# Performance work log

Hardware: AMD Instinct MI355X
Metric: run time of the kernel (lower is better)

Reference implementation:

```python
import jax, jax.numpy as jnp
import numpy as np

B, T, E, H = 4, 4096, 1024, 16
D = E // H          # per-head hidden_size in fla LinearAttention (num_heads=1)
CH = 64             # fused-chunk chunk size


def setup_inputs() -> dict:
    key = jax.random.key(0)
    k1, k2, k3, k4, k5 = jax.random.split(key, 5)
    s = 1.0 / np.sqrt(D).astype(np.float32)
    x = jax.random.normal(k1, (B, T, E), dtype=jnp.float32)
    Wq = jax.random.normal(k2, (D, D), dtype=jnp.float32) * s
    Wk = jax.random.normal(k3, (D, D), dtype=jnp.float32) * s
    Wv = jax.random.normal(k4, (D, D), dtype=jnp.float32) * s
    Wo = jax.random.normal(k5, (D, D), dtype=jnp.float32) * s
    return {"x": x, "Wq": Wq, "Wk": Wk, "Wv": Wv, "Wo": Wo}


def _phi(x):
    # fla 'elu' feature map: elu(x) + 1 (positive features)
    return jax.nn.elu(x) + 1.0


def _linear_attn_fused_chunk(q, k, v):
    # q,k,v: [B,H,T,D]; causal linear attention via chunked recurrence.
    b, h, t, d = q.shape
    n = t // CH
    # [N, B, H, CH, D] so scan runs over chunks
    qc = q.reshape(b, h, n, CH, d).transpose(2, 0, 1, 3, 4)
    kc = k.reshape(b, h, n, CH, d).transpose(2, 0, 1, 3, 4)
    vc = v.reshape(b, h, n, CH, d).transpose(2, 0, 1, 3, 4)
    mask = jnp.tril(jnp.ones((CH, CH), dtype=q.dtype))  # causal, diag inclusive

    def step(S, inp):
        qi, ki, vi = inp                                   # [B,H,CH,D]
        attn = jnp.einsum('bhck,bhek->bhce', qi, ki) * mask  # intra-chunk scores
        o_intra = jnp.einsum('bhce,bhed->bhcd', attn, vi)
        o_inter = jnp.einsum('bhck,bhkd->bhcd', qi, S)       # past-state term
        S_new = S + jnp.einsum('bhck,bhcd->bhkd', ki, vi)    # state update
        return S_new, o_intra + o_inter

    S0 = jnp.zeros((b, h, d, d), dtype=q.dtype)
    _, oc = jax.lax.scan(step, S0, (qc, kc, vc))           # oc: [N,B,H,CH,D]
    return oc.transpose(1, 2, 0, 3, 4).reshape(b, h, t, d)


def reference(x, Wq, Wk, Wv, Wo):
    # split outer heads: [B,T,E] -> [B,H,T,D]
    xh = x.reshape(B, T, H, D).transpose(0, 2, 1, 3)
    # shared [D,D] projections (fla LinearAttention with num_heads=1), tied elu feature map on q,k
    q = _phi(jnp.einsum('bhtd,de->bhte', xh, Wq))
    k = _phi(jnp.einsum('bhtd,de->bhte', xh, Wk))
    v = jnp.einsum('bhtd,de->bhte', xh, Wv)
    o = _linear_attn_fused_chunk(q, k, v)                  # no feature-map norm, identity output norm
    o = jnp.einsum('bhtd,de->bhte', o, Wo)
    return o.transpose(0, 2, 1, 3).reshape(B, T, E)
```

## Files before the change

kernel.cpp:

```cpp
#include <hip/hip_runtime.h>
#include <cstdint>
#include <cstddef>

constexpr int Bc = 4, Tc = 4096, Ec = 1024, Hc = 16, Dc = 64, CHc = 64;
constexpr int NSEG = 16;
constexpr int SEGT = Tc / NSEG;
constexpr int NCHUNK = SEGT / CHc;

typedef __attribute__((ext_vector_type(8))) short short8;
typedef __attribute__((ext_vector_type(4))) float f32x4;

__device__ __forceinline__ unsigned short* sws(unsigned short* b, int row, int colbyte) {
  return (unsigned short*)((char*)b + (row << 7) + (colbyte ^ ((row & 7) << 4)));
}

__device__ __forceinline__ unsigned short f2bf(float f) {
  union { float f; unsigned int u; } v; v.f = f;
  return (unsigned short)((v.u + 0x7FFFu + ((v.u >> 16) & 1u)) >> 16);
}
__device__ __forceinline__ unsigned int pk2(float lo, float hi) {
  union { float f; unsigned int u; } a, b; a.f = lo; b.f = hi;
  return ((a.u + 0x8000u) >> 16) | ((b.u + 0x8000u) & 0xFFFF0000u);
}
__device__ __forceinline__ float bf2f(unsigned short u) {
  union { unsigned int u; float f; } v; v.u = ((unsigned int)u) << 16;
  return v.f;
}
__device__ __forceinline__ float phi_elu1(float x) {
  return x > 0.f ? x + 1.f : __expf(x);
}
__device__ __forceinline__ short8 ld8(const unsigned short* p) {
  return *reinterpret_cast<const short8*>(p);
}
__device__ __forceinline__ short8 pk8(float4 a, float4 b) {
  union { unsigned int u[4]; short8 s; } r;
  r.u[0] = pk2(a.x, a.y); r.u[1] = pk2(a.z, a.w);
  r.u[2] = pk2(b.x, b.y); r.u[3] = pk2(b.z, b.w);
  return r.s;
}
__device__ __forceinline__ void st4(unsigned short* p, float v0, float v1, float v2, float v3) {
  uint2 t; t.x = pk2(v0, v1); t.y = pk2(v2, v3);
  *reinterpret_cast<uint2*>(p) = t;
}

#define MFMA(a, b, c) __builtin_amdgcn_mfma_f32_16x16x32_bf16((a), (b), (c), 0, 0, 0)

__global__ __launch_bounds__(256) void prep_weights(
    const float* __restrict__ Wq, const float* __restrict__ Wk,
    const float* __restrict__ Wv, const float* __restrict__ Wo,
    unsigned short* __restrict__ wbuf) {
  __shared__ float s_wvT[4096];
  __shared__ float s_wo[4096];
  const int tid = threadIdx.x;
  const int i = blockIdx.x * 256 + tid;
  for (int j = tid; j < 4096; j += 256) {
    s_wvT[(j & 63) * 64 + (j >> 6)] = Wv[j];
    s_wo[j] = Wo[j];
  }
  __syncthreads();
  const int r = i >> 6, c = i & 63;
  wbuf[c * 64 + r] = f2bf(Wq[i]);
  wbuf[4096 + c * 64 + r] = f2bf(Wk[i]);
  float acc = 0.f;
  for (int g = 0; g < 64; ++g)
    acc += s_wvT[g * 64 + c] * s_wo[g * 64 + r];
  wbuf[8192 + i] = f2bf(acc);
}

__global__ __launch_bounds__(256, 3) void pass1_kvseg(
    const float* __restrict__ x, const unsigned short* __restrict__ wbuf,
    float* __restrict__ kvseg) {
  __shared__ unsigned short s_kT[4096];
  __shared__ unsigned short s_vT[4096];
  const int tid = threadIdx.x, w = tid >> 6, lane = tid & 63, lr = lane & 15, lq = lane >> 4;
  const int bh = blockIdx.x, sg = blockIdx.y, b = bh >> 4, h = bh & 15;
  const float* xbase = x + ((size_t)b * Tc + (size_t)sg * SEGT) * Ec + h * Dc;
  const unsigned short* wkT = wbuf + 4096;
  const unsigned short* wvoT = wbuf + 8192;
  const f32x4 Z = {0.f, 0.f, 0.f, 0.f};

  short8 bwk[4][2], bwv[4][2];
#pragma unroll
  for (int c = 0; c < 4; ++c)
#pragma unroll
    for (int kk = 0; kk < 2; ++kk) {
      bwk[c][kk] = ld8(wkT + (c * 16 + lr) * 64 + kk * 32 + lq * 8);
      bwv[c][kk] = ld8(wvoT + (c * 16 + lr) * 64 + kk * 32 + lq * 8);
    }

  const float* xr = xbase + (size_t)(w * 16 + lr) * Ec + lq * 8;
  float4 p0 = ((const float4*)xr)[0], p1 = ((const float4*)xr)[1];
  float4 p2 = ((const float4*)(xr + 32))[0], p3 = ((const float4*)(xr + 32))[1];

  f32x4 sacc[4] = {Z, Z, Z, Z};
#pragma unroll
  for (int ci = 0; ci < NCHUNK; ++ci) {
    short8 xa0 = pk8(p0, p1), xa1 = pk8(p2, p3);
    if (ci < NCHUNK - 1) {
      const float* nr = xbase + (size_t)((ci + 1) * CHc + w * 16 + lr) * Ec + lq * 8;
      p0 = ((const float4*)nr)[0]; p1 = ((const float4*)nr)[1];
      p2 = ((const float4*)(nr + 32))[0]; p3 = ((const float4*)(nr + 32))[1];
    }
    f32x4 ak[4] = {Z, Z, Z, Z}, av[4] = {Z, Z, Z, Z};
#pragma unroll
    for (int c = 0; c < 4; ++c) {
      ak[c] = MFMA(xa0, bwk[c][0], ak[c]); ak[c] = MFMA(xa1, bwk[c][1], ak[c]);
      av[c] = MFMA(xa0, bwv[c][0], av[c]); av[c] = MFMA(xa1, bwv[c][1], av[c]);
    }
#pragma unroll
    for (int c = 0; c < 4; ++c) {
      unsigned short* pk_ = sws(s_kT, c * 16 + lr, w * 32 + lq * 8);
      unsigned short* pv_ = sws(s_vT, c * 16 + lr, w * 32 + lq * 8);
      st4(pk_, phi_elu1(ak[c][0]), phi_elu1(ak[c][1]), phi_elu1(ak[c][2]), phi_elu1(ak[c][3]));
      st4(pv_, av[c][0], av[c][1], av[c][2], av[c][3]);
    }
    __syncthreads();

    short8 akt0 = ld8(sws(s_kT, w * 16 + lr, lq * 16));
    short8 akt1 = ld8(sws(s_kT, w * 16 + lr, 64 + lq * 16));
#pragma unroll
    for (int c = 0; c < 4; ++c) {
      sacc[c] = MFMA(akt0, ld8(sws(s_vT, c * 16 + lr, lq * 16)), sacc[c]);
      sacc[c] = MFMA(akt1, ld8(sws(s_vT, c * 16 + lr, 64 + lq * 16)), sacc[c]);
    }
    __syncthreads();
  }
  float* dst = kvseg + ((size_t)(bh * NSEG + sg)) * 4096;
#pragma unroll
  for (int c = 0; c < 4; ++c)
#pragma unroll
    for (int j = 0; j < 4; ++j)
      dst[(w * 16 + lq * 4 + j) * 64 + c * 16 + lr] = sacc[c][j];
}

__global__ __launch_bounds__(256) void pass2_prefix(const float* __restrict__ kvseg,
                                                    unsigned short* __restrict__ sprefix) {
  const int bh = blockIdx.x, tile = blockIdx.y;
  const int e = tile * 1024 + threadIdx.x * 4;
  const float* src = kvseg + (size_t)bh * NSEG * 4096 + e;
  unsigned short* dst = sprefix + (size_t)bh * NSEG * 4096 + e;
  float4 vals[NSEG];
#pragma unroll
  for (int s = 0; s < NSEG; ++s) vals[s] = *(const float4*)(src + (size_t)s * 4096);
  float a0 = 0.f, a1 = 0.f, a2 = 0.f, a3 = 0.f;
#pragma unroll
  for (int s = 0; s < NSEG; ++s) {
    uint2 t; t.x = pk2(a0, a1); t.y = pk2(a2, a3);
    *reinterpret_cast<uint2*>(dst + (size_t)s * 4096) = t;
    a0 += vals[s].x; a1 += vals[s].y; a2 += vals[s].z; a3 += vals[s].w;
  }
}

__global__ __launch_bounds__(256, 2) void pass3_main(
    const float* __restrict__ x, const unsigned short* __restrict__ wbuf,
    const unsigned short* __restrict__ sprefix, float* __restrict__ out) {
  __shared__ unsigned short s_x [4096];
  __shared__ unsigned short s_q [4096];
  __shared__ unsigned short s_k [4096];
  __shared__ unsigned short s_kT[4096];
  __shared__ unsigned short s_vT[4096];
  __shared__ unsigned short s_Sb[4096];

  const int tid = threadIdx.x, w = tid >> 6, lane = tid & 63, lr = lane & 15, lq = lane >> 4;
  const int bh = blockIdx.x, sg = blockIdx.y, b = bh >> 4, h = bh & 15;
  const float* xbase = x + ((size_t)b * Tc + (size_t)sg * SEGT) * Ec + h * Dc;
  float* obase = out + ((size_t)b * Tc + (size_t)sg * SEGT) * Ec + h * Dc;
  const unsigned short* wqT = wbuf;
  const unsigned short* wkT = wbuf + 4096;
  const unsigned short* wvoT = wbuf + 8192;
  const unsigned short* Sg = sprefix + ((size_t)(bh * NSEG + sg)) * 4096;
  const int sr = tid >> 2, sc = tid & 3;
  const f32x4 Z = {0.f, 0.f, 0.f, 0.f};

  f32x4 sacc[4];
#pragma unroll
  for (int c = 0; c < 4; ++c)
#pragma unroll
    for (int j = 0; j < 4; ++j)
      sacc[c][j] = bf2f(Sg[(w * 16 + lq * 4 + j) * 64 + c * 16 + lr]);

  short8 awq[2], awk[2], bwk[4][2], bwv[4][2];
#pragma unroll
  for (int kk = 0; kk < 2; ++kk) {
    awq[kk] = ld8(wqT + (w * 16 + lr) * 64 + kk * 32 + lq * 8);
    awk[kk] = ld8(wkT + (w * 16 + lr) * 64 + kk * 32 + lq * 8);
  }
#pragma unroll
  for (int c = 0; c < 4; ++c)
#pragma unroll
    for (int kk = 0; kk < 2; ++kk) {
      bwk[c][kk] = ld8(wkT + (c * 16 + lr) * 64 + kk * 32 + lq * 8);
      bwv[c][kk] = ld8(wvoT + (c * 16 + lr) * 64 + kk * 32 + lq * 8);
    }

  {
    const float4* xf = (const float4*)(xbase + (size_t)sr * Ec + sc * 16);
    float4 f0 = xf[0], f1 = xf[1], f2 = xf[2], f3 = xf[3];
    *(short8*)sws(s_x, sr, sc * 32) = pk8(f0, f1);
    *(short8*)sws(s_x, sr, sc * 32 + 16) = pk8(f2, f3);
  }
  __syncthreads();

#pragma unroll
  for (int ci = 0; ci < NCHUNK; ++ci) {
    float4 pf0, pf1, pf2, pf3;
    if (ci < NCHUNK - 1) {
      const float4* xf = (const float4*)(xbase + (size_t)((ci + 1) * CHc + sr) * Ec + sc * 16);
      pf0 = xf[0]; pf1 = xf[1]; pf2 = xf[2]; pf3 = xf[3];
    }

    short8 xb[4][2];
#pragma unroll
    for (int c = 0; c < 4; ++c) {
      xb[c][0] = ld8(sws(s_x, c * 16 + lr, lq * 16));
      xb[c][1] = ld8(sws(s_x, c * 16 + lr, 64 + lq * 16));
    }
    short8 xw0 = ld8(sws(s_x, w * 16 + lr, lq * 16));
    short8 xw1 = ld8(sws(s_x, w * 16 + lr, 64 + lq * 16));
#pragma unroll
    for (int c = 0; c < 4; ++c)
      st4(sws(s_Sb, c * 16 + lr, w * 32 + lq * 8), sacc[c][0], sacc[c][1], sacc[c][2], sacc[c][3]);

    f32x4 aqt[4] = {Z, Z, Z, Z}, akt[4] = {Z, Z, Z, Z}, ack[4] = {Z, Z, Z, Z}, acv[4] = {Z, Z, Z, Z};
#pragma unroll
    for (int c = 0; c < 4; ++c) {
      aqt[c] = MFMA(awq[0], xb[c][0], aqt[c]); aqt[c] = MFMA(awq[1], xb[c][1], aqt[c]);
      akt[c] = MFMA(awk[0], xb[c][0], akt[c]); akt[c] = MFMA(awk[1], xb[c][1], akt[c]);
      ack[c] = MFMA(xw0, bwk[c][0], ack[c]);   ack[c] = MFMA(xw1, bwk[c][1], ack[c]);
      acv[c] = MFMA(xw0, bwv[c][0], acv[c]);   acv[c] = MFMA(xw1, bwv[c][1], acv[c]);
    }
#pragma unroll
    for (int c = 0; c < 4; ++c) {
      const int row = c * 16 + lr, cb = w * 32 + lq * 8;
      st4(sws(s_q, row, cb), phi_elu1(aqt[c][0]), phi_elu1(aqt[c][1]), phi_elu1(aqt[c][2]), phi_elu1(aqt[c][3]));
      st4(sws(s_k, row, cb), phi_elu1(akt[c][0]), phi_elu1(akt[c][1]), phi_elu1(akt[c][2]), phi_elu1(akt[c][3]));
      st4(sws(s_kT, row, cb), phi_elu1(ack[c][0]), phi_elu1(ack[c][1]), phi_elu1(ack[c][2]), phi_elu1(ack[c][3]));
      st4(sws(s_vT, row, cb), acv[c][0], acv[c][1], acv[c][2], acv[c][3]);
    }
    __syncthreads();

    short8 a_q0 = ld8(sws(s_q, w * 16 + lr, lq * 16));
    short8 a_q1 = ld8(sws(s_q, w * 16 + lr, 64 + lq * 16));
    short8 a_k0 = ld8(sws(s_k, w * 16 + lr, lq * 16));
    short8 a_k1 = ld8(sws(s_k, w * 16 + lr, 64 + lq * 16));
    short8 a_t0 = ld8(sws(s_kT, w * 16 + lr, lq * 16));
    short8 a_t1 = ld8(sws(s_kT, w * 16 + lr, 64 + lq * 16));
    f32x4 aat[4] = {Z, Z, Z, Z}, ao[4] = {Z, Z, Z, Z};
#pragma unroll
    for (int c = 0; c < 4; ++c) {
      const int row = c * 16 + lr;
      aat[c]  = MFMA(a_k0, ld8(sws(s_q, row, lq * 16)), aat[c]);
      aat[c]  = MFMA(a_k1, ld8(sws(s_q, row, 64 + lq * 16)), aat[c]);
      ao[c]   = MFMA(a_q0, ld8(sws(s_Sb, row, lq * 16)), ao[c]);
      ao[c]   = MFMA(a_q1, ld8(sws(s_Sb, row, 64 + lq * 16)), ao[c]);
      sacc[c] = MFMA(a_t0, ld8(sws(s_vT, row, lq * 16)), sacc[c]);
      sacc[c] = MFMA(a_t1, ld8(sws(s_vT, row, 64 + lq * 16)), sacc[c]);
    }
#pragma unroll
    for (int c = 0; c < 4; ++c) {
      int t = c * 16 + lr, tp = w * 16 + lq * 4;
      float m0 = (tp + 0 <= t) ? aat[c][0] : 0.f;
      float m1 = (tp + 1 <= t) ? aat[c][1] : 0.f;
      float m2 = (tp + 2 <= t) ? aat[c][2] : 0.f;
      float m3 = (tp + 3 <= t) ? aat[c][3] : 0.f;
      st4(sws(s_x, t, tp * 2), m0, m1, m2, m3);
    }
    __syncthreads();

    short8 a_a0 = ld8(sws(s_x, w * 16 + lr, lq * 16));
    short8 a_a1 = ld8(sws(s_x, w * 16 + lr, 64 + lq * 16));
#pragma unroll
    for (int c = 0; c < 4; ++c) {
      const int row = c * 16 + lr;
      ao[c] = MFMA(a_a0, ld8(sws(s_vT, row, lq * 16)), ao[c]);
      ao[c] = MFMA(a_a1, ld8(sws(s_vT, row, 64 + lq * 16)), ao[c]);
    }
    float* orow = obase + (size_t)(ci * CHc) * Ec;
#pragma unroll
    for (int c = 0; c < 4; ++c)
#pragma unroll
      for (int j = 0; j < 4; ++j)
        orow[(size_t)(w * 16 + lq * 4 + j) * Ec + c * 16 + lr] = ao[c][j];
    if (ci < NCHUNK - 1) {
      *(short8*)sws(s_x, sr, sc * 32) = pk8(pf0, pf1);
      *(short8*)sws(s_x, sr, sc * 32 + 16) = pk8(pf2, pf3);
    }
    __syncthreads();
  }
}

extern "C" void kernel_launch(void* const* d_in, const int* in_sizes, int n_in,
                              void* d_out, int out_size, void* d_ws, size_t ws_size,
                              hipStream_t stream) {
  const float* x  = (const float*)d_in[0];
  const float* Wq = (const float*)d_in[1];
  const float* Wk = (const float*)d_in[2];
  const float* Wv = (const float*)d_in[3];
  const float* Wo = (const float*)d_in[4];
  float* out = (float*)d_out;

  unsigned short* wbuf = (unsigned short*)d_ws;
  float* kvseg = (float*)((char*)d_ws + 32768);
  unsigned short* sprefix = (unsigned short*)((char*)d_ws + 32768 + (size_t)16 * 1024 * 1024);

  prep_weights<<<dim3(16), dim3(256), 0, stream>>>(Wq, Wk, Wv, Wo, wbuf);
  pass1_kvseg<<<dim3(64, NSEG), dim3(256), 0, stream>>>(x, wbuf, kvseg);
  pass2_prefix<<<dim3(64, 4), dim3(256), 0, stream>>>(kvseg, sprefix);
  pass3_main<<<dim3(64, NSEG), dim3(256), 0, stream>>>(x, wbuf, sprefix, out);
}
```

Measured before the change: 77.56 us.

## Split pass1 into half-segment blocks, double pass3 waves, store kv partials in bf16

Pass1 now computes KV partial sums over two-chunk half-segments (32 per head) and stores them in bf16 with a transposed layout. Pass2 reads these bf16 partials and writes the prefix only at even indices. Pass3 runs with 512 threads, each wave covering half the column tiles, and double-buffers the x tile in shared memory. It also loads fewer weight fragments per thread. The aim is more parallelism and less partial-sum traffic, at the cost of bf16 rounding in the partials and extra LDS use.

```diff
diff --git a/kernel.cpp b/kernel.cpp
--- a/kernel.cpp
+++ b/kernel.cpp
@@ -6,6 +6,7 @@
 constexpr int NSEG = 16;
 constexpr int SEGT = Tc / NSEG;
 constexpr int NCHUNK = SEGT / CHc;
+constexpr int NHALF = 32;
 
 typedef __attribute__((ext_vector_type(8))) short short8;
 typedef __attribute__((ext_vector_type(4))) float f32x4;
@@ -20,10 +21,10 @@
 }
 __device__ __forceinline__ unsigned int pk2(float lo, float hi) {
   union { float f; unsigned int u; } a, b; a.f = lo; b.f = hi;
-  return ((a.u + 0x8000u) >> 16) | ((b.u + 0x8000u) & 0xFFFF0000u);
-}
-__device__ __forceinline__ float bf2f(unsigned short u) {
-  union { unsigned int u; float f; } v; v.u = ((unsigned int)u) << 16;
+  return __builtin_amdgcn_perm(b.u + 0x8000u, a.u + 0x8000u, 0x07060302u);
+}
+__device__ __forceinline__ float bf2f(unsigned int u16) {
+  union { unsigned int u; float f; } v; v.u = u16 << 16;
   return v.f;
 }
 __device__ __forceinline__ float phi_elu1(float x) {
@@ -67,14 +68,14 @@
   wbuf[8192 + i] = f2bf(acc);
 }
 
-__global__ __launch_bounds__(256, 3) void pass1_kvseg(
+__global__ __launch_bounds__(256, 3) void pass1_kvhalf(
     const float* __restrict__ x, const unsigned short* __restrict__ wbuf,
-    float* __restrict__ kvseg) {
+    unsigned short* __restrict__ kvh) {
   __shared__ unsigned short s_kT[4096];
   __shared__ unsigned short s_vT[4096];
   const int tid = threadIdx.x, w = tid >> 6, lane = tid & 63, lr = lane & 15, lq = lane >> 4;
-  const int bh = blockIdx.x, sg = blockIdx.y, b = bh >> 4, h = bh & 15;
-  const float* xbase = x + ((size_t)b * Tc + (size_t)sg * SEGT) * Ec + h * Dc;
+  const int bh = blockIdx.x, hs = blockIdx.y, b = bh >> 4, h = bh & 15;
+  const float* xbase = x + ((size_t)b * Tc + (size_t)hs * 2 * CHc) * Ec + h * Dc;
   const unsigned short* wkT = wbuf + 4096;
   const unsigned short* wvoT = wbuf + 8192;
   const f32x4 Z = {0.f, 0.f, 0.f, 0.f};
@@ -94,10 +95,10 @@
 
   f32x4 sacc[4] = {Z, Z, Z, Z};
 #pragma unroll
-  for (int ci = 0; ci < NCHUNK; ++ci) {
+  for (int ci = 0; ci < 2; ++ci) {
     short8 xa0 = pk8(p0, p1), xa1 = pk8(p2, p3);
-    if (ci < NCHUNK - 1) {
-      const float* nr = xbase + (size_t)((ci + 1) * CHc + w * 16 + lr) * Ec + lq * 8;
+    if (ci == 0) {
+      const float* nr = xbase + (size_t)(CHc + w * 16 + lr) * Ec + lq * 8;
       p0 = ((const float4*)nr)[0]; p1 = ((const float4*)nr)[1];
       p2 = ((const float4*)(nr + 32))[0]; p3 = ((const float4*)(nr + 32))[1];
     }
@@ -109,13 +110,11 @@
     }
 #pragma unroll
     for (int c = 0; c < 4; ++c) {
-      unsigned short* pk_ = sws(s_kT, c * 16 + lr, w * 32 + lq * 8);
-      unsigned short* pv_ = sws(s_vT, c * 16 + lr, w * 32 + lq * 8);
-      st4(pk_, phi_elu1(ak[c][0]), phi_elu1(ak[c][1]), phi_elu1(ak[c][2]), phi_elu1(ak[c][3]));
-      st4(pv_, av[c][0], av[c][1], av[c][2], av[c][3]);
-    }
-    __syncthreads();
-
+      st4(sws(s_kT, c * 16 + lr, w * 32 + lq * 8),
+          phi_elu1(ak[c][0]), phi_elu1(ak[c][1]), phi_elu1(ak[c][2]), phi_elu1(ak[c][3]));
+      st4(sws(s_vT, c * 16 + lr, w * 32 + lq * 8), av[c][0], av[c][1], av[c][2], av[c][3]);
+    }
+    __syncthreads();
     short8 akt0 = ld8(sws(s_kT, w * 16 + lr, lq * 16));
     short8 akt1 = ld8(sws(s_kT, w * 16 + lr, 64 + lq * 16));
 #pragma unroll
@@ -125,36 +124,39 @@
     }
     __syncthreads();
   }
-  float* dst = kvseg + ((size_t)(bh * NSEG + sg)) * 4096;
-#pragma unroll
-  for (int c = 0; c < 4; ++c)
-#pragma unroll
-    for (int j = 0; j < 4; ++j)
-      dst[(w * 16 + lq * 4 + j) * 64 + c * 16 + lr] = sacc[c][j];
-}
-
-__global__ __launch_bounds__(256) void pass2_prefix(const float* __restrict__ kvseg,
-                                                    unsigned short* __restrict__ sprefix) {
+  unsigned short* dst = kvh + ((size_t)bh * NHALF + hs) * 4096;
+#pragma unroll
+  for (int c = 0; c < 4; ++c) {
+    uint2 t; t.x = pk2(sacc[c][0], sacc[c][1]); t.y = pk2(sacc[c][2], sacc[c][3]);
+    *reinterpret_cast<uint2*>(dst + (c * 16 + lr) * 64 + w * 16 + lq * 4) = t;
+  }
+}
+
+__global__ __launch_bounds__(256) void pass2_prefix(const unsigned short* __restrict__ kvh,
+                                                    unsigned short* __restrict__ spre) {
   const int bh = blockIdx.x, tile = blockIdx.y;
-  const int e = tile * 1024 + threadIdx.x * 4;
-  const float* src = kvseg + (size_t)bh * NSEG * 4096 + e;
-  unsigned short* dst = sprefix + (size_t)bh * NSEG * 4096 + e;
-  float4 vals[NSEG];
-#pragma unroll
-  for (int s = 0; s < NSEG; ++s) vals[s] = *(const float4*)(src + (size_t)s * 4096);
+  const int e4 = tile * 1024 + threadIdx.x * 4;
+  const unsigned short* src = kvh + (size_t)bh * NHALF * 4096 + e4;
+  unsigned short* dst = spre + (size_t)bh * NSEG * 4096 + e4;
+  uint2 vals[NHALF];
+#pragma unroll
+  for (int s = 0; s < NHALF; ++s) vals[s] = *(const uint2*)(src + (size_t)s * 4096);
   float a0 = 0.f, a1 = 0.f, a2 = 0.f, a3 = 0.f;
 #pragma unroll
-  for (int s = 0; s < NSEG; ++s) {
-    uint2 t; t.x = pk2(a0, a1); t.y = pk2(a2, a3);
-    *reinterpret_cast<uint2*>(dst + (size_t)s * 4096) = t;
-    a0 += vals[s].x; a1 += vals[s].y; a2 += vals[s].z; a3 += vals[s].w;
-  }
-}
-
-__global__ __launch_bounds__(256, 2) void pass3_main(
+  for (int s = 0; s < NHALF; ++s) {
+    if ((s & 1) == 0) {
+      uint2 t; t.x = pk2(a0, a1); t.y = pk2(a2, a3);
+      *reinterpret_cast<uint2*>(dst + (size_t)(s >> 1) * 4096) = t;
+    }
+    a0 += bf2f(vals[s].x & 0xFFFFu); a1 += bf2f(vals[s].x >> 16);
+    a2 += bf2f(vals[s].y & 0xFFFFu); a3 += bf2f(vals[s].y >> 16);
+  }
+}
+
+__global__ __launch_bounds__(512, 2) void pass3_main(
     const float* __restrict__ x, const unsigned short* __restrict__ wbuf,
-    const unsigned short* __restrict__ sprefix, float* __restrict__ out) {
-  __shared__ unsigned short s_x [4096];
+    const unsigned short* __restrict__ spre, float* __restrict__ out) {
+  __shared__ unsigned short s_xb[2][4096];
   __shared__ unsigned short s_q [4096];
   __shared__ unsigned short s_k [4096];
   __shared__ unsigned short s_kT[4096];
@@ -162,129 +164,137 @@
   __shared__ unsigned short s_Sb[4096];
 
   const int tid = threadIdx.x, w = tid >> 6, lane = tid & 63, lr = lane & 15, lq = lane >> 4;
+  const int wr = w & 3, wc = w >> 2;
+  const int sr8 = tid >> 3, sc8 = tid & 7;
   const int bh = blockIdx.x, sg = blockIdx.y, b = bh >> 4, h = bh & 15;
   const float* xbase = x + ((size_t)b * Tc + (size_t)sg * SEGT) * Ec + h * Dc;
   float* obase = out + ((size_t)b * Tc + (size_t)sg * SEGT) * Ec + h * Dc;
   const unsigned short* wqT = wbuf;
   const unsigned short* wkT = wbuf + 4096;
   const unsigned short* wvoT = wbuf + 8192;
-  const unsigned short* Sg = sprefix + ((size_t)(bh * NSEG + sg)) * 4096;
-  const int sr = tid >> 2, sc = tid & 3;
+  const unsigned short* SgT = spre + ((size_t)(bh * NSEG + sg)) * 4096;
   const f32x4 Z = {0.f, 0.f, 0.f, 0.f};
 
-  f32x4 sacc[4];
-#pragma unroll
-  for (int c = 0; c < 4; ++c)
-#pragma unroll
-    for (int j = 0; j < 4; ++j)
-      sacc[c][j] = bf2f(Sg[(w * 16 + lq * 4 + j) * 64 + c * 16 + lr]);
-
-  short8 awq[2], awk[2], bwk[4][2], bwv[4][2];
+  const int rA = wr * 16 + lr;
+  const int r0 = (2 * wc) * 16 + lr;
+  const int r1 = (2 * wc + 1) * 16 + lr;
+
+  f32x4 sacc[2];
+  {
+    uint2 u0 = *(const uint2*)(SgT + r0 * 64 + wr * 16 + lq * 4);
+    uint2 u1 = *(const uint2*)(SgT + r1 * 64 + wr * 16 + lq * 4);
+    sacc[0][0] = bf2f(u0.x & 0xFFFFu); sacc[0][1] = bf2f(u0.x >> 16);
+    sacc[0][2] = bf2f(u0.y & 0xFFFFu); sacc[0][3] = bf2f(u0.y >> 16);
+    sacc[1][0] = bf2f(u1.x & 0xFFFFu); sacc[1][1] = bf2f(u1.x >> 16);
+    sacc[1][2] = bf2f(u1.y & 0xFFFFu); sacc[1][3] = bf2f(u1.y >> 16);
+  }
+
+  short8 awq[2], awk[2], bwk[2][2], bwv[2][2];
 #pragma unroll
   for (int kk = 0; kk < 2; ++kk) {
-    awq[kk] = ld8(wqT + (w * 16 + lr) * 64 + kk * 32 + lq * 8);
-    awk[kk] = ld8(wkT + (w * 16 + lr) * 64 + kk * 32 + lq * 8);
-  }
-#pragma unroll
-  for (int c = 0; c < 4; ++c)
+    awq[kk] = ld8(wqT + rA * 64 + kk * 32 + lq * 8);
+    awk[kk] = ld8(wkT + rA * 64 + kk * 32 + lq * 8);
+    bwk[0][kk] = ld8(wkT + r0 * 64 + kk * 32 + lq * 8);
+    bwk[1][kk] = ld8(wkT + r1 * 64 + kk * 32 + lq * 8);
+    bwv[0][kk] = ld8(wvoT + r0 * 64 + kk * 32 + lq * 8);
+    bwv[1][kk] = ld8(wvoT + r1 * 64 + kk * 32 + lq * 8);
+  }
+
+  {
+    const float4* xf = (const float4*)(xbase + (size_t)sr8 * Ec + sc8 * 8);
+    *(short8*)sws(s_xb[0], sr8, sc8 * 16) = pk8(xf[0], xf[1]);
+  }
+  __syncthreads();
+
+#pragma unroll
+  for (int ci = 0; ci < NCHUNK; ++ci) {
+    unsigned short* cur = s_xb[ci & 1];
+    unsigned short* nxt = s_xb[(ci & 1) ^ 1];
+
+    short8 xb0[2], xb1[2], xw[2];
 #pragma unroll
     for (int kk = 0; kk < 2; ++kk) {
-      bwk[c][kk] = ld8(wkT + (c * 16 + lr) * 64 + kk * 32 + lq * 8);
-      bwv[c][kk] = ld8(wvoT + (c * 16 + lr) * 64 + kk * 32 + lq * 8);
-    }
-
-  {
-    const float4* xf = (const float4*)(xbase + (size_t)sr * Ec + sc * 16);
-    float4 f0 = xf[0], f1 = xf[1], f2 = xf[2], f3 = xf[3];
-    *(short8*)sws(s_x, sr, sc * 32) = pk8(f0, f1);
-    *(short8*)sws(s_x, sr, sc * 32 + 16) = pk8(f2, f3);
-  }
-  __syncthreads();
-
-#pragma unroll
-  for (int ci = 0; ci < NCHUNK; ++ci) {
-    float4 pf0, pf1, pf2, pf3;
+      xb0[kk] = ld8(sws(cur, r0, kk * 64 + lq * 16));
+      xb1[kk] = ld8(sws(cur, r1, kk * 64 + lq * 16));
+      xw[kk]  = ld8(sws(cur, rA, kk * 64 + lq * 16));
+    }
+    st4(sws(s_Sb, r0, wr * 32 + lq * 8), sacc[0][0], sacc[0][1], sacc[0][2], sacc[0][3]);
+    st4(sws(s_Sb, r1, wr * 32 + lq * 8), sacc[1][0], sacc[1][1], sacc[1][2], sacc[1][3]);
+
+    f32x4 aqt[2] = {Z, Z}, akt[2] = {Z, Z}, ack[2] = {Z, Z}, acv[2] = {Z, Z};
+    aqt[0] = MFMA(awq[0], xb0[0], aqt[0]); aqt[0] = MFMA(awq[1], xb0[1], aqt[0]);
+    aqt[1] = MFMA(awq[0], xb1[0], aqt[1]); aqt[1] = MFMA(awq[1], xb1[1], aqt[1]);
+    akt[0] = MFMA(awk[0], xb0[0], akt[0]); akt[0] = MFMA(awk[1], xb0[1], akt[0]);
+    akt[1] = MFMA(awk[0], xb1[0], akt[1]); akt[1] = MFMA(awk[1], xb1[1], akt[1]);
+    ack[0] = MFMA(xw[0], bwk[0][0], ack[0]); ack[0] = MFMA(xw[1], bwk[0][1], ack[0]);
+    ack[1] = MFMA(xw[0], bwk[1][0], ack[1]); ack[1] = MFMA(xw[1], bwk[1][1], ack[1]);
+    acv[0] = MFMA(xw[0], bwv[0][0], acv[0]); acv[0] = MFMA(xw[1], bwv[0][1], acv[0]);
+    acv[1] = MFMA(xw[0], bwv[1][0], acv[1]); acv[1] = MFMA(xw[1], bwv[1][1], acv[1]);
+
+#pragma unroll
+    for (int c2 = 0; c2 < 2; ++c2) {
+      const int row = c2 ? r1 : r0, cb = wr * 32 + lq * 8;
+      st4(sws(s_q, row, cb), phi_elu1(aqt[c2][0]), phi_elu1(aqt[c2][1]), phi_elu1(aqt[c2][2]), phi_elu1(aqt[c2][3]));
+      st4(sws(s_k, row, cb), phi_elu1(akt[c2][0]), phi_elu1(akt[c2][1]), phi_elu1(akt[c2][2]), phi_elu1(akt[c2][3]));
+      st4(sws(s_kT, row, cb), phi_elu1(ack[c2][0]), phi_elu1(ack[c2][1]), phi_elu1(ack[c2][2]), phi_elu1(ack[c2][3]));
+      st4(sws(s_vT, row, cb), acv[c2][0], acv[c2][1], acv[c2][2], acv[c2][3]);
+    }
+    __syncthreads();
+
+    float4 pf0, pf1;
     if (ci < NCHUNK - 1) {
-      const float4* xf = (const float4*)(xbase + (size_t)((ci + 1) * CHc + sr) * Ec + sc * 16);
-      pf0 = xf[0]; pf1 = xf[1]; pf2 = xf[2]; pf3 = xf[3];
-    }
-
-    short8 xb[4][2];
-#pragma unroll
-    for (int c = 0; c < 4; ++c) {
-      xb[c][0] = ld8(sws(s_x, c * 16 + lr, lq * 16));
-      xb[c][1] = ld8(sws(s_x, c * 16 + lr, 64 + lq * 16));
-    }
-    short8 xw0 = ld8(sws(s_x, w * 16 + lr, lq * 16));
-    short8 xw1 = ld8(sws(s_x, w * 16 + lr, 64 + lq * 16));
-#pragma unroll
-    for (int c = 0; c < 4; ++c)
-      st4(sws(s_Sb, c * 16 + lr, w * 32 + lq * 8), sacc[c][0], sacc[c][1], sacc[c][2], sacc[c][3]);
-
-    f32x4 aqt[4] = {Z, Z, Z, Z}, akt[4] = {Z, Z, Z, Z}, ack[4] = {Z, Z, Z, Z}, acv[4] = {Z, Z, Z, Z};
-#pragma unroll
-    for (int c = 0; c < 4; ++c) {
-      aqt[c] = MFMA(awq[0], xb[c][0], aqt[c]); aqt[c] = MFMA(awq[1], xb[c][1], aqt[c]);
-      akt[c] = MFMA(awk[0], xb[c][0], akt[c]); akt[c] = MFMA(awk[1], xb[c][1], akt[c]);
-      ack[c] = MFMA(xw0, bwk[c][0], ack[c]);   ack[c] = MFMA(xw1, bwk[c][1], ack[c]);
-      acv[c] = MFMA(xw0, bwv[c][0], acv[c]);   acv[c] = MFMA(xw1, bwv[c][1], acv[c]);
-    }
-#pragma unroll
-    for (int c = 0; c < 4; ++c) {
-      const int row = c * 16 + lr, cb = w * 32 + lq * 8;
-      st4(sws(s_q, row, cb), phi_elu1(aqt[c][0]), phi_elu1(aqt[c][1]), phi_elu1(aqt[c][2]), phi_elu1(aqt[c][3]));
-      st4(sws(s_k, row, cb), phi_elu1(akt[c][0]), phi_elu1(akt[c][1]), phi_elu1(akt[c][2]), phi_elu1(akt[c][3]));
-      st4(sws(s_kT, row, cb), phi_elu1(ack[c][0]), phi_elu1(ack[c][1]), phi_elu1(ack[c][2]), phi_elu1(ack[c][3]));
-      st4(sws(s_vT, row, cb), acv[c][0], acv[c][1], acv[c][2], acv[c][3]);
-    }
-    __syncthreads();
-
-    short8 a_q0 = ld8(sws(s_q, w * 16 + lr, lq * 16));
-    short8 a_q1 = ld8(sws(s_q, w * 16 + lr, 64 + lq * 16));
-    short8 a_k0 = ld8(sws(s_k, w * 16 + lr, lq * 16));
-    short8 a_k1 = ld8(sws(s_k, w * 16 + lr, 64 + lq * 16));
-    short8 a_t0 = ld8(sws(s_kT, w * 16 + lr, lq * 16));
-    short8 a_t1 = ld8(sws(s_kT, w * 16 + lr, 64 + lq * 16));
-    f32x4 aat[4] = {Z, Z, Z, Z}, ao[4] = {Z, Z, Z, Z};
-#pragma unroll
-    for (int c = 0; c < 4; ++c) {
-      const int row = c * 16 + lr;
-      aat[c]  = MFMA(a_k0, ld8(sws(s_q, row, lq * 16)), aat[c]);
-      aat[c]  = MFMA(a_k1, ld8(sws(s_q, row, 64 + lq * 16)), aat[c]);
-      ao[c]   = MFMA(a_q0, ld8(sws(s_Sb, row, lq * 16)), ao[c]);
-      ao[c]   = MFMA(a_q1, ld8(sws(s_Sb, row, 64 + lq * 16)), ao[c]);
-      sacc[c] = MFMA(a_t0, ld8(sws(s_vT, row, lq * 16)), sacc[c]);
-      sacc[c] = MFMA(a_t1, ld8(sws(s_vT, row, 64 + lq * 16)), sacc[c]);
-    }
-#pragma unroll
-    for (int c = 0; c < 4; ++c) {
-      int t = c * 16 + lr, tp = w * 16 + lq * 4;
-      float m0 = (tp + 0 <= t) ? aat[c][0] : 0.f;
-      float m1 = (tp + 1 <= t) ? aat[c][1] : 0.f;
-      float m2 = (tp + 2 <= t) ? aat[c][2] : 0.f;
-      float m3 = (tp + 3 <= t) ? aat[c][3] : 0.f;
-      st4(sws(s_x, t, tp * 2), m0, m1, m2, m3);
-    }
-    __syncthreads();
-
-    short8 a_a0 = ld8(sws(s_x, w * 16 + lr, lq * 16));
-    short8 a_a1 = ld8(sws(s_x, w * 16 + lr, 64 + lq * 16));
-#pragma unroll
-    for (int c = 0; c < 4; ++c) {
-      const int row = c * 16 + lr;
-      ao[c] = MFMA(a_a0, ld8(sws(s_vT, row, lq * 16)), ao[c]);
-      ao[c] = MFMA(a_a1, ld8(sws(s_vT, row, 64 + lq * 16)), ao[c]);
+      const float4* xf = (const float4*)(xbase + (size_t)((ci + 1) * CHc + sr8) * Ec + sc8 * 8);
+      pf0 = xf[0]; pf1 = xf[1];
+    }
+
+    short8 aq[2], ak2[2], at[2];
+#pragma unroll
+    for (int kk = 0; kk < 2; ++kk) {
+      aq[kk]  = ld8(sws(s_q, rA, kk * 64 + lq * 16));
+      ak2[kk] = ld8(sws(s_k, rA, kk * 64 + lq * 16));
+      at[kk]  = ld8(sws(s_kT, rA, kk * 64 + lq * 16));
+    }
+    f32x4 aat[2] = {Z, Z}, ao[2] = {Z, Z};
+#pragma unroll
+    for (int c2 = 0; c2 < 2; ++c2) {
+      const int row = c2 ? r1 : r0;
+      aat[c2]  = MFMA(ak2[0], ld8(sws(s_q, row, lq * 16)), aat[c2]);
+      aat[c2]  = MFMA(ak2[1], ld8(sws(s_q, row, 64 + lq * 16)), aat[c2]);
+      ao[c2]   = MFMA(aq[0], ld8(sws(s_Sb, row, lq * 16)), ao[c2]);
+      ao[c2]   = MFMA(aq[1], ld8(sws(s_Sb, row, 64 + lq * 16)), ao[c2]);
+      sacc[c2] = MFMA(at[0], ld8(sws(s_vT, row, lq * 16)), sacc[c2]);
+      sacc[c2] = MFMA(at[1], ld8(sws(s_vT, row, 64 + lq * 16)), sacc[c2]);
+    }
+#pragma unroll
+    for (int c2 = 0; c2 < 2; ++c2) {
+      const int t = c2 ? r1 : r0, tp = wr * 16 + lq * 4;
+      float m0 = (tp + 0 <= t) ? aat[c2][0] : 0.f;
+      float m1 = (tp + 1 <= t) ? aat[c2][1] : 0.f;
+      float m2 = (tp + 2 <= t) ? aat[c2][2] : 0.f;
+      float m3 = (tp + 3 <= t) ? aat[c2][3] : 0.f;
+      st4(sws(cur, t, tp * 2), m0, m1, m2, m3);
+    }
+    __syncthreads();
+
+    short8 aa[2];
+    aa[0] = ld8(sws(cur, rA, lq * 16));
+    aa[1] = ld8(sws(cur, rA, 64 + lq * 16));
+#pragma unroll
+    for (int c2 = 0; c2 < 2; ++c2) {
+      const int row = c2 ? r1 : r0;
+      ao[c2] = MFMA(aa[0], ld8(sws(s_vT, row, lq * 16)), ao[c2]);
+      ao[c2] = MFMA(aa[1], ld8(sws(s_vT, row, 64 + lq * 16)), ao[c2]);
     }
     float* orow = obase + (size_t)(ci * CHc) * Ec;
 #pragma unroll
-    for (int c = 0; c < 4; ++c)
+    for (int c2 = 0; c2 < 2; ++c2) {
+      const int col = c2 ? r1 : r0;
 #pragma unroll
       for (int j = 0; j < 4; ++j)
-        orow[(size_t)(w * 16 + lq * 4 + j) * Ec + c * 16 + lr] = ao[c][j];
-    if (ci < NCHUNK - 1) {
-      *(short8*)sws(s_x, sr, sc * 32) = pk8(pf0, pf1);
-      *(short8*)sws(s_x, sr, sc * 32 + 16) = pk8(pf2, pf3);
-    }
+        orow[(size_t)(wr * 16 + lq * 4 + j) * Ec + col] = ao[c2][j];
+    }
+    if (ci < NCHUNK - 1)
+      *(short8*)sws(nxt, sr8, sc8 * 16) = pk8(pf0, pf1);
     __syncthreads();
   }
 }
@@ -300,11 +310,11 @@
   float* out = (float*)d_out;
 
   unsigned short* wbuf = (unsigned short*)d_ws;
-  float* kvseg = (float*)((char*)d_ws + 32768);
-  unsigned short* sprefix = (unsigned short*)((char*)d_ws + 32768 + (size_t)16 * 1024 * 1024);
+  unsigned short* kvh  = (unsigned short*)((char*)d_ws + 32768);
+  unsigned short* spre = (unsigned short*)((char*)d_ws + 32768 + (size_t)16 * 1024 * 1024);
 
   prep_weights<<<dim3(16), dim3(256), 0, stream>>>(Wq, Wk, Wv, Wo, wbuf);
-  pass1_kvseg<<<dim3(64, NSEG), dim3(256), 0, stream>>>(x, wbuf, kvseg);
-  pass2_prefix<<<dim3(64, 4), dim3(256), 0, stream>>>(kvseg, sprefix);
-  pass3_main<<<dim3(64, NSEG), dim3(256), 0, stream>>>(x, wbuf, sprefix, out);
-}
+  pass1_kvhalf<<<dim3(64, NHALF), dim3(256), 0, stream>>>(x, wbuf, kvh);
+  pass2_prefix<<<dim3(64, 4), dim3(256), 0, stream>>>(kvh, spre);
+  pass3_main<<<dim3(64, NSEG), dim3(512), 0, stream>>>(x, wbuf, spre, out);
+}
```

New measurement: 89.13 us. 14.9% more time.

## Compute per-chunk KV states in pass1 and scan them in bf16 prefix pass

Applied to the files above, without the earlier changes.

Pass1 now launches one block per 64-token chunk instead of per 256-token segment, so there is no serial chunk loop and the grid is four times larger. It writes each chunk's K^T V state as bf16 in a register-fragment layout. Pass2 scans all 64 chunk states, emitting bf16 segment prefixes, and pass3 reads them with vectorized loads in that fragment layout. The diff also adds s_setprio around the MFMA blocks in pass3 and a perm-based bf16 pack; bf16 storage of the per-chunk partials adds rounding error to the accumulation.

```diff
diff --git a/kernel.cpp b/kernel.cpp
--- a/kernel.cpp
+++ b/kernel.cpp
@@ -6,6 +6,7 @@
 constexpr int NSEG = 16;
 constexpr int SEGT = Tc / NSEG;
 constexpr int NCHUNK = SEGT / CHc;
+constexpr int NCH = Tc / CHc;
 
 typedef __attribute__((ext_vector_type(8))) short short8;
 typedef __attribute__((ext_vector_type(4))) float f32x4;
@@ -20,10 +21,10 @@
 }
 __device__ __forceinline__ unsigned int pk2(float lo, float hi) {
   union { float f; unsigned int u; } a, b; a.f = lo; b.f = hi;
-  return ((a.u + 0x8000u) >> 16) | ((b.u + 0x8000u) & 0xFFFF0000u);
-}
-__device__ __forceinline__ float bf2f(unsigned short u) {
-  union { unsigned int u; float f; } v; v.u = ((unsigned int)u) << 16;
+  return __builtin_amdgcn_perm(b.u + 0x8000u, a.u + 0x8000u, 0x07060302u);
+}
+__device__ __forceinline__ float bf2f(unsigned int u16) {
+  union { unsigned int u; float f; } v; v.u = u16 << 16;
   return v.f;
 }
 __device__ __forceinline__ float phi_elu1(float x) {
@@ -67,14 +68,14 @@
   wbuf[8192 + i] = f2bf(acc);
 }
 
-__global__ __launch_bounds__(256, 3) void pass1_kvseg(
+__global__ __launch_bounds__(256, 3) void pass1_kvchunk(
     const float* __restrict__ x, const unsigned short* __restrict__ wbuf,
-    float* __restrict__ kvseg) {
+    unsigned short* __restrict__ kvc) {
   __shared__ unsigned short s_kT[4096];
   __shared__ unsigned short s_vT[4096];
   const int tid = threadIdx.x, w = tid >> 6, lane = tid & 63, lr = lane & 15, lq = lane >> 4;
-  const int bh = blockIdx.x, sg = blockIdx.y, b = bh >> 4, h = bh & 15;
-  const float* xbase = x + ((size_t)b * Tc + (size_t)sg * SEGT) * Ec + h * Dc;
+  const int bh = blockIdx.x, ch = blockIdx.y, b = bh >> 4, h = bh & 15;
+  const float* xbase = x + ((size_t)b * Tc + (size_t)ch * CHc) * Ec + h * Dc;
   const unsigned short* wkT = wbuf + 4096;
   const unsigned short* wvoT = wbuf + 8192;
   const f32x4 Z = {0.f, 0.f, 0.f, 0.f};
@@ -91,69 +92,68 @@
   const float* xr = xbase + (size_t)(w * 16 + lr) * Ec + lq * 8;
   float4 p0 = ((const float4*)xr)[0], p1 = ((const float4*)xr)[1];
   float4 p2 = ((const float4*)(xr + 32))[0], p3 = ((const float4*)(xr + 32))[1];
-
+  short8 xa0 = pk8(p0, p1), xa1 = pk8(p2, p3);
+
+  f32x4 ak[4] = {Z, Z, Z, Z}, av[4] = {Z, Z, Z, Z};
+#pragma unroll
+  for (int c = 0; c < 4; ++c) {
+    ak[c] = MFMA(xa0, bwk[c][0], ak[c]); ak[c] = MFMA(xa1, bwk[c][1], ak[c]);
+    av[c] = MFMA(xa0, bwv[c][0], av[c]); av[c] = MFMA(xa1, bwv[c][1], av[c]);
+  }
+#pragma unroll
+  for (int c = 0; c < 4; ++c) {
+    st4(sws(s_kT, c * 16 + lr, w * 32 + lq * 8),
+        phi_elu1(ak[c][0]), phi_elu1(ak[c][1]), phi_elu1(ak[c][2]), phi_elu1(ak[c][3]));
+    st4(sws(s_vT, c * 16 + lr, w * 32 + lq * 8), av[c][0], av[c][1], av[c][2], av[c][3]);
+  }
+  __syncthreads();
+
+  short8 akt0 = ld8(sws(s_kT, w * 16 + lr, lq * 16));
+  short8 akt1 = ld8(sws(s_kT, w * 16 + lr, 64 + lq * 16));
   f32x4 sacc[4] = {Z, Z, Z, Z};
 #pragma unroll
-  for (int ci = 0; ci < NCHUNK; ++ci) {
-    short8 xa0 = pk8(p0, p1), xa1 = pk8(p2, p3);
-    if (ci < NCHUNK - 1) {
-      const float* nr = xbase + (size_t)((ci + 1) * CHc + w * 16 + lr) * Ec + lq * 8;
-      p0 = ((const float4*)nr)[0]; p1 = ((const float4*)nr)[1];
-      p2 = ((const float4*)(nr + 32))[0]; p3 = ((const float4*)(nr + 32))[1];
-    }
-    f32x4 ak[4] = {Z, Z, Z, Z}, av[4] = {Z, Z, Z, Z};
-#pragma unroll
-    for (int c = 0; c < 4; ++c) {
-      ak[c] = MFMA(xa0, bwk[c][0], ak[c]); ak[c] = MFMA(xa1, bwk[c][1], ak[c]);
-      av[c] = MFMA(xa0, bwv[c][0], av[c]); av[c] = MFMA(xa1, bwv[c][1], av[c]);
-    }
-#pragma unroll
-    for (int c = 0; c < 4; ++c) {
-      unsigned short* pk_ = sws(s_kT, c * 16 + lr, w * 32 + lq * 8);
-      unsigned short* pv_ = sws(s_vT, c * 16 + lr, w * 32 + lq * 8);
-      st4(pk_, phi_elu1(ak[c][0]), phi_elu1(ak[c][1]), phi_elu1(ak[c][2]), phi_elu1(ak[c][3]));
-      st4(pv_, av[c][0], av[c][1], av[c][2], av[c][3]);
-    }
-    __syncthreads();
-
-    short8 akt0 = ld8(sws(s_kT, w * 16 + lr, lq * 16));
-    short8 akt1 = ld8(sws(s_kT, w * 16 + lr, 64 + lq * 16));
-#pragma unroll
-    for (int c = 0; c < 4; ++c) {
-      sacc[c] = MFMA(akt0, ld8(sws(s_vT, c * 16 + lr, lq * 16)), sacc[c]);
-      sacc[c] = MFMA(akt1, ld8(sws(s_vT, c * 16 + lr, 64 + lq * 16)), sacc[c]);
-    }
-    __syncthreads();
-  }
-  float* dst = kvseg + ((size_t)(bh * NSEG + sg)) * 4096;
-#pragma unroll
-  for (int c = 0; c < 4; ++c)
-#pragma unroll
-    for (int j = 0; j < 4; ++j)
-      dst[(w * 16 + lq * 4 + j) * 64 + c * 16 + lr] = sacc[c][j];
-}
-
-__global__ __launch_bounds__(256) void pass2_prefix(const float* __restrict__ kvseg,
-                                                    unsigned short* __restrict__ sprefix) {
-  const int bh = blockIdx.x, tile = blockIdx.y;
-  const int e = tile * 1024 + threadIdx.x * 4;
-  const float* src = kvseg + (size_t)bh * NSEG * 4096 + e;
-  unsigned short* dst = sprefix + (size_t)bh * NSEG * 4096 + e;
-  float4 vals[NSEG];
-#pragma unroll
-  for (int s = 0; s < NSEG; ++s) vals[s] = *(const float4*)(src + (size_t)s * 4096);
+  for (int c = 0; c < 4; ++c) {
+    sacc[c] = MFMA(akt0, ld8(sws(s_vT, c * 16 + lr, lq * 16)), sacc[c]);
+    sacc[c] = MFMA(akt1, ld8(sws(s_vT, c * 16 + lr, 64 + lq * 16)), sacc[c]);
+  }
+
+  unsigned short* dst = kvc + ((size_t)bh * NCH + ch) * 4096 + (w * 64 + lane) * 16;
+#pragma unroll
+  for (int c = 0; c < 4; ++c) {
+    uint2 t; t.x = pk2(sacc[c][0], sacc[c][1]); t.y = pk2(sacc[c][2], sacc[c][3]);
+    *reinterpret_cast<uint2*>(dst + c * 4) = t;
+  }
+}
+
+__global__ __launch_bounds__(256) void pass2_prefix(const unsigned short* __restrict__ kvc,
+                                                    unsigned short* __restrict__ spre) {
+  const int bh = blockIdx.x, tb = blockIdx.y;
+  const int slot = tb * 256 + threadIdx.x;
+  const unsigned short* src = kvc + (size_t)bh * NCH * 4096 + slot * 4;
+  unsigned short* dst = spre + (size_t)bh * NSEG * 4096 + slot * 4;
   float a0 = 0.f, a1 = 0.f, a2 = 0.f, a3 = 0.f;
 #pragma unroll
-  for (int s = 0; s < NSEG; ++s) {
-    uint2 t; t.x = pk2(a0, a1); t.y = pk2(a2, a3);
-    *reinterpret_cast<uint2*>(dst + (size_t)s * 4096) = t;
-    a0 += vals[s].x; a1 += vals[s].y; a2 += vals[s].z; a3 += vals[s].w;
+  for (int base = 0; base < NCH; base += 8) {
+    uint2 v[8];
+#pragma unroll
+    for (int i = 0; i < 8; ++i)
+      v[i] = *reinterpret_cast<const uint2*>(src + (size_t)(base + i) * 4096);
+#pragma unroll
+    for (int i = 0; i < 8; ++i) {
+      const int c = base + i;
+      if ((c & 3) == 0) {
+        uint2 t; t.x = pk2(a0, a1); t.y = pk2(a2, a3);
+        *reinterpret_cast<uint2*>(dst + (size_t)(c >> 2) * 4096) = t;
+      }
+      a0 += bf2f(v[i].x & 0xFFFFu); a1 += bf2f(v[i].x >> 16);
+      a2 += bf2f(v[i].y & 0xFFFFu); a3 += bf2f(v[i].y >> 16);
+    }
   }
 }
 
 __global__ __launch_bounds__(256, 2) void pass3_main(
     const float* __restrict__ x, const unsigned short* __restrict__ wbuf,
-    const unsigned short* __restrict__ sprefix, float* __restrict__ out) {
+    const unsigned short* __restrict__ spre, float* __restrict__ out) {
   __shared__ unsigned short s_x [4096];
   __shared__ unsigned short s_q [4096];
   __shared__ unsigned short s_k [4096];
@@ -168,16 +168,19 @@
   const unsigned short* wqT = wbuf;
   const unsigned short* wkT = wbuf + 4096;
   const unsigned short* wvoT = wbuf + 8192;
-  const unsigned short* Sg = sprefix + ((size_t)(bh * NSEG + sg)) * 4096;
   const int sr = tid >> 2, sc = tid & 3;
   const f32x4 Z = {0.f, 0.f, 0.f, 0.f};
 
   f32x4 sacc[4];
-#pragma unroll
-  for (int c = 0; c < 4; ++c)
-#pragma unroll
-    for (int j = 0; j < 4; ++j)
-      sacc[c][j] = bf2f(Sg[(w * 16 + lq * 4 + j) * 64 + c * 16 + lr]);
+  {
+    const unsigned short* Sg = spre + ((size_t)(bh * NSEG + sg)) * 4096 + (w * 64 + lane) * 16;
+#pragma unroll
+    for (int c = 0; c < 4; ++c) {
+      uint2 u = *reinterpret_cast<const uint2*>(Sg + c * 4);
+      sacc[c][0] = bf2f(u.x & 0xFFFFu); sacc[c][1] = bf2f(u.x >> 16);
+      sacc[c][2] = bf2f(u.y & 0xFFFFu); sacc[c][3] = bf2f(u.y >> 16);
+    }
+  }
 
   short8 awq[2], awk[2], bwk[4][2], bwv[4][2];
 #pragma unroll
@@ -222,6 +225,7 @@
       st4(sws(s_Sb, c * 16 + lr, w * 32 + lq * 8), sacc[c][0], sacc[c][1], sacc[c][2], sacc[c][3]);
 
     f32x4 aqt[4] = {Z, Z, Z, Z}, akt[4] = {Z, Z, Z, Z}, ack[4] = {Z, Z, Z, Z}, acv[4] = {Z, Z, Z, Z};
+    __builtin_amdgcn_s_setprio(1);
 #pragma unroll
     for (int c = 0; c < 4; ++c) {
       aqt[c] = MFMA(awq[0], xb[c][0], aqt[c]); aqt[c] = MFMA(awq[1], xb[c][1], aqt[c]);
@@ -229,6 +233,7 @@
       ack[c] = MFMA(xw0, bwk[c][0], ack[c]);   ack[c] = MFMA(xw1, bwk[c][1], ack[c]);
       acv[c] = MFMA(xw0, bwv[c][0], acv[c]);   acv[c] = MFMA(xw1, bwv[c][1], acv[c]);
     }
+    __builtin_amdgcn_s_setprio(0);
 #pragma unroll
     for (int c = 0; c < 4; ++c) {
       const int row = c * 16 + lr, cb = w * 32 + lq * 8;
@@ -246,6 +251,7 @@
     short8 a_t0 = ld8(sws(s_kT, w * 16 + lr, lq * 16));
     short8 a_t1 = ld8(sws(s_kT, w * 16 + lr, 64 + lq * 16));
     f32x4 aat[4] = {Z, Z, Z, Z}, ao[4] = {Z, Z, Z, Z};
+    __builtin_amdgcn_s_setprio(1);
 #pragma unroll
     for (int c = 0; c < 4; ++c) {
       const int row = c * 16 + lr;
@@ -256,6 +262,7 @@
       sacc[c] = MFMA(a_t0, ld8(sws(s_vT, row, lq * 16)), sacc[c]);
       sacc[c] = MFMA(a_t1, ld8(sws(s_vT, row, 64 + lq * 16)), sacc[c]);
     }
+    __builtin_amdgcn_s_setprio(0);
 #pragma unroll
     for (int c = 0; c < 4; ++c) {
       int t = c * 16 + lr, tp = w * 16 + lq * 4;
@@ -269,12 +276,14 @@
 
     short8 a_a0 = ld8(sws(s_x, w * 16 + lr, lq * 16));
     short8 a_a1 = ld8(sws(s_x, w * 16 + lr, 64 + lq * 16));
+    __builtin_amdgcn_s_setprio(1);
 #pragma unroll
     for (int c = 0; c < 4; ++c) {
       const int row = c * 16 + lr;
       ao[c] = MFMA(a_a0, ld8(sws(s_vT, row, lq * 16)), ao[c]);
       ao[c] = MFMA(a_a1, ld8(sws(s_vT, row, 64 + lq * 16)), ao[c]);
     }
+    __builtin_amdgcn_s_setprio(0);
     float* orow = obase + (size_t)(ci * CHc) * Ec;
 #pragma unroll
     for (int c = 0; c < 4; ++c)
@@ -300,11 +309,11 @@
   float* out = (float*)d_out;
 
   unsigned short* wbuf = (unsigned short*)d_ws;
-  float* kvseg = (float*)((char*)d_ws + 32768);
-  unsigned short* sprefix = (unsigned short*)((char*)d_ws + 32768 + (size_t)16 * 1024 * 1024);
+  unsigned short* kvc  = (unsigned short*)((char*)d_ws + 32768);
+  unsigned short* spre = (unsigned short*)((char*)d_ws + 32768 + (size_t)32 * 1024 * 1024);
 
   prep_weights<<<dim3(16), dim3(256), 0, stream>>>(Wq, Wk, Wv, Wo, wbuf);
-  pass1_kvseg<<<dim3(64, NSEG), dim3(256), 0, stream>>>(x, wbuf, kvseg);
-  pass2_prefix<<<dim3(64, 4), dim3(256), 0, stream>>>(kvseg, sprefix);
-  pass3_main<<<dim3(64, NSEG), dim3(256), 0, stream>>>(x, wbuf, sprefix, out);
-}
+  pass1_kvchunk<<<dim3(64, NCH), dim3(256), 0, stream>>>(x, wbuf, kvc);
+  pass2_prefix<<<dim3(64, 4), dim3(256), 0, stream>>>(kvc, spre);
+  pass3_main<<<dim3(64, NSEG), dim3(256), 0, stream>>>(x, wbuf, spre, out);
+}
```

Result: slower. 94.28 us (+21.6%).
